# Kernel optimization log

Hardware: AMD Instinct MI355X
Metric: run time of the kernel (lower is better)

The kernel has to match this reference:

```python
import jax, jax.numpy as jnp
import numpy as np

N = 32768        # tokens (batch*seq)
D = 1024         # input_dim
E = 64           # n_experts
TOPK = 2


def setup_inputs() -> dict:
    key = jax.random.key(0)
    k_x, k_w, k_b, k_wn, k_bn = jax.random.split(key, 5)
    scale = 1.0 / np.sqrt(D)
    return {
        "x": jax.random.normal(k_x, (N, D), dtype=jnp.float32),
        "W": jax.random.uniform(k_w, (D, E), minval=-scale, maxval=scale, dtype=jnp.float32),
        "b": jax.random.uniform(k_b, (E,), minval=-scale, maxval=scale, dtype=jnp.float32),
        "W_noise": jax.random.uniform(k_wn, (D, E), minval=-scale, maxval=scale, dtype=jnp.float32),
        "b_noise": jax.random.uniform(k_bn, (E,), minval=-scale, maxval=scale, dtype=jnp.float32),
    }


def reference(x, W, b, W_noise, b_noise):
    # logits = fc(x): single Linear (router_hidden_dims=[])
    logits = x @ W + b                      # [N, E]
    # training=False (default): no noise path; fc_noise params unused
    topk_logits, topk_indices = jax.lax.top_k(logits, TOPK)  # [N, k]
    # scatter topk logits into a -inf tensor, then softmax
    mask = jnp.sum(jax.nn.one_hot(topk_indices, E, dtype=jnp.bool_), axis=-2)  # [N, E]
    sparse_logits = jnp.where(mask, logits, -jnp.inf)
    routing_probs = jax.nn.softmax(sparse_logits, axis=-1)  # zeros off-topk
    return routing_probs, topk_indices
```

## Files before the change

kernel.cpp:

```cpp
#include <hip/hip_runtime.h>
#include <cstdint>
#include <cstddef>

#define N_TOK 32768
#define DIM   1024
#define NE    64
#define RPB   64
#define KHALF 512
#define CHUNK 32
#define NCHUNK (KHALF / CHUNK)

__device__ __forceinline__ void gload16(const float* g, float* l) {
  __builtin_amdgcn_global_load_lds(
      (const __attribute__((address_space(1))) uint32_t*)g,
      (__attribute__((address_space(3))) uint32_t*)l, 16, 0, 0);
}

__global__ __launch_bounds__(512, 4) void router_kernel(
    const float* __restrict__ x, const float* __restrict__ W,
    const float* __restrict__ bias, float* __restrict__ probs,
    float* __restrict__ idxo) {
  __shared__ __align__(1024) float xs[2][2][RPB][CHUNK];
  __shared__ float  red[4][RPB][16];
  __shared__ float4 ex[4][RPB];
  __shared__ float4 ex2[RPB];

  const int tid  = threadIdx.x;
  const int lane = tid & 63;
  const int w    = __builtin_amdgcn_readfirstlane(tid >> 6);
  const int g    = w & 3;
  const int h    = w >> 2;
  const int r0   = blockIdx.x * RPB;

  auto stage = [&](int cc) {
    const int buf = cc & 1;
    float* base = &xs[h][buf][0][0];
    const int k0 = h * KHALF + cc * CHUNK;
#pragma unroll
    for (int jj = 0; jj < 2; ++jj) {
      const int j = 2 * g + jj;
      const int row = 8 * j + (lane >> 3);
      const int sq  = (lane & 7) ^ (lane >> 3);
      gload16(x + (size_t)(r0 + row) * DIM + k0 + (sq << 2),
              base + j * 256);
    }
  };

  float acc[16];
#pragma unroll
  for (int e = 0; e < 16; ++e) acc[e] = 0.0f;

  stage(0);

  for (int cc = 0; cc < NCHUNK; ++cc) {
    __syncthreads();
    if (cc + 1 < NCHUNK) stage(cc + 1);

    const int buf = cc & 1;
    const float* xb = &xs[h][buf][0][0] + lane * CHUNK;
    const float* Wc = W + (size_t)(h * KHALF + cc * CHUNK) * NE + g * 16;

    float4 xq = make_float4(0.f, 0.f, 0.f, 0.f);
#pragma unroll
    for (int kk = 0; kk < CHUNK; ++kk) {
      if ((kk & 3) == 0) {
        const int slot = (kk >> 2) ^ (lane & 7);
        xq = *(const float4*)(xb + (slot << 2));
      }
      const float xc = ((kk & 3) == 0) ? xq.x
                     : ((kk & 3) == 1) ? xq.y
                     : ((kk & 3) == 2) ? xq.z : xq.w;
      const float* Wk = Wc + (size_t)kk * NE;
#pragma unroll
      for (int e = 0; e < 16; ++e)
        acc[e] = fmaf(Wk[e], xc, acc[e]);
    }
  }

  __syncthreads();
  if (h == 1) {
#pragma unroll
    for (int q = 0; q < 4; ++q)
      *(float4*)&red[g][lane][q * 4] = make_float4(acc[q*4+0], acc[q*4+1],
                                                   acc[q*4+2], acc[q*4+3]);
  }
  __syncthreads();

  if (h == 0) {
#pragma unroll
    for (int q = 0; q < 4; ++q) {
      float4 r = *(const float4*)&red[g][lane][q * 4];
      acc[q*4+0] += r.x; acc[q*4+1] += r.y; acc[q*4+2] += r.z; acc[q*4+3] += r.w;
    }
#pragma unroll
    for (int e = 0; e < 16; ++e) acc[e] += bias[g * 16 + e];

    float v1, v2; int j1, j2;
    if (acc[1] > acc[0]) { v1 = acc[1]; j1 = 1; v2 = acc[0]; j2 = 0; }
    else                 { v1 = acc[0]; j1 = 0; v2 = acc[1]; j2 = 1; }
#pragma unroll
    for (int e = 2; e < 16; ++e) {
      if (acc[e] > v1)      { v2 = v1; j2 = j1; v1 = acc[e]; j1 = e; }
      else if (acc[e] > v2) { v2 = acc[e]; j2 = e; }
    }
    ex[g][lane] = make_float4(v1, v2, (float)(g * 16 + j1), (float)(g * 16 + j2));
  }
  __syncthreads();

  if (w == 0) {
    float4 m = ex[0][lane];
    float V1 = m.x, V2 = m.y, J1 = m.z, J2 = m.w;
#pragma unroll
    for (int gg = 1; gg < 4; ++gg) {
      float4 u = ex[gg][lane];
      if (u.x > V1) {
        bool s = (u.y > V1);
        V2 = s ? u.y : V1; J2 = s ? u.w : J1;
        V1 = u.x; J1 = u.z;
      } else if (u.x > V2) { V2 = u.x; J2 = u.z; }
    }
    const float e2 = __expf(V2 - V1);
    const float p1 = 1.0f / (1.0f + e2);
    const float p2 = e2 * p1;
    ex2[lane] = make_float4(J1, J2, p1, p2);
    float2 oi; oi.x = J1; oi.y = J2;
    *(float2*)(idxo + (size_t)(r0 + lane) * 2) = oi;
  }
  __syncthreads();

  if (h == 0) {
    float4 f = ex2[lane];
    const int ij1 = (int)f.x, ij2 = (int)f.y;
    float* op = probs + (size_t)(r0 + lane) * NE + g * 16;
#pragma unroll
    for (int q = 0; q < 4; ++q) {
      float4 o;
      const int e0 = g * 16 + q * 4;
      o.x = (e0 + 0 == ij1) ? f.z : (e0 + 0 == ij2) ? f.w : 0.0f;
      o.y = (e0 + 1 == ij1) ? f.z : (e0 + 1 == ij2) ? f.w : 0.0f;
      o.z = (e0 + 2 == ij1) ? f.z : (e0 + 2 == ij2) ? f.w : 0.0f;
      o.w = (e0 + 3 == ij1) ? f.z : (e0 + 3 == ij2) ? f.w : 0.0f;
      *(float4*)(op + q * 4) = o;
    }
  }
}

extern "C" void kernel_launch(void* const* d_in, const int* in_sizes, int n_in,
                              void* d_out, int out_size, void* d_ws, size_t ws_size,
                              hipStream_t stream) {
  (void)in_sizes; (void)n_in; (void)out_size; (void)d_ws; (void)ws_size;
  const float* x = (const float*)d_in[0];
  const float* W = (const float*)d_in[1];
  const float* b = (const float*)d_in[2];
  float* out  = (float*)d_out;
  float* idxo = out + (size_t)N_TOK * NE;

  dim3 grid(N_TOK / RPB);
  dim3 block(512);
  hipLaunchKernelGGL(router_kernel, grid, block, 0, stream, x, W, b, out, idxo);
}
```

Before: 248.2 us.

## Use 8x8 register tiles with split-K across waves and LDS-staged W

Replaces the per-lane row dot product, where each lane reads W directly from global memory, with an 8-row by 8-expert register tile per lane. Both x, transposed with an XOR swizzle, and W chunks are double-buffered in LDS, and each of the 8 waves handles a different slice of K. Partial sums are combined through a tree reduction in shared memory, and wave 0 does the top-2 selection using cross-lane shuffles. The aim is to raise FMA-to-load ratio and cut redundant W traffic. In exchange it uses 64 accumulators per lane and adds several extra barriers, which adds register pressure and may lower occupancy.

```diff
diff --git a/kernel.cpp b/kernel.cpp
--- a/kernel.cpp
+++ b/kernel.cpp
@@ -6,9 +6,8 @@
 #define DIM   1024
 #define NE    64
 #define RPB   64
-#define KHALF 512
-#define CHUNK 32
-#define NCHUNK (KHALF / CHUNK)
+#define CH    64
+#define NCH   (DIM / CH)
 
 __device__ __forceinline__ void gload16(const float* g, float* l) {
   __builtin_amdgcn_global_load_lds(
@@ -20,127 +19,193 @@
     const float* __restrict__ x, const float* __restrict__ W,
     const float* __restrict__ bias, float* __restrict__ probs,
     float* __restrict__ idxo) {
-  __shared__ __align__(1024) float xs[2][2][RPB][CHUNK];
-  __shared__ float  red[4][RPB][16];
-  __shared__ float4 ex[4][RPB];
-  __shared__ float4 ex2[RPB];
+  __shared__ __align__(1024) float smem[16384];
+  float* xT = smem;
+  float* wB = smem + 8192;
 
   const int tid  = threadIdx.x;
   const int lane = tid & 63;
   const int w    = __builtin_amdgcn_readfirstlane(tid >> 6);
-  const int g    = w & 3;
-  const int h    = w >> 2;
+  const int ri   = lane >> 3;
+  const int ei   = lane & 7;
   const int r0   = blockIdx.x * RPB;
 
-  auto stage = [&](int cc) {
+  const int srow = tid >> 3;
+  const int sq   = tid & 7;
+  const float* xrow = x + (size_t)(r0 + srow) * DIM + sq * 4;
+
+  float acc[64];
+#pragma unroll
+  for (int i = 0; i < 64; ++i) acc[i] = 0.0f;
+
+  const int rp0 = srow ^ ((sq >> 1) << 3);
+  const int rp1 = srow ^ ((((sq + 8) >> 1)) << 3);
+
+  float4 xg0 = *(const float4*)(xrow);
+  float4 xg1 = *(const float4*)(xrow + 32);
+#pragma unroll
+  for (int jj = 0; jj < 2; ++jj) {
+    const int j = w * 2 + jj;
+    gload16(W + (size_t)(j * 4) * NE + lane * 4, wB + j * 256);
+  }
+  {
+    float* xb = xT;
+    const int q1 = sq + 8;
+    xb[(sq*4+0)*64 + rp0] = xg0.x;  xb[(sq*4+1)*64 + rp0] = xg0.y;
+    xb[(sq*4+2)*64 + rp0] = xg0.z;  xb[(sq*4+3)*64 + rp0] = xg0.w;
+    xb[(q1*4+0)*64 + rp1] = xg1.x;  xb[(q1*4+1)*64 + rp1] = xg1.y;
+    xb[(q1*4+2)*64 + rp1] = xg1.z;  xb[(q1*4+3)*64 + rp1] = xg1.w;
+  }
+
+  for (int cc = 0; cc < NCH; ++cc) {
+    __syncthreads();
     const int buf = cc & 1;
-    float* base = &xs[h][buf][0][0];
-    const int k0 = h * KHALF + cc * CHUNK;
-#pragma unroll
-    for (int jj = 0; jj < 2; ++jj) {
-      const int j = 2 * g + jj;
-      const int row = 8 * j + (lane >> 3);
-      const int sq  = (lane & 7) ^ (lane >> 3);
-      gload16(x + (size_t)(r0 + row) * DIM + k0 + (sq << 2),
-              base + j * 256);
+    const int nb  = buf ^ 1;
+    const bool pf = (cc + 1 < NCH);
+
+    if (pf) {
+      const int k0n = (cc + 1) * CH;
+      xg0 = *(const float4*)(xrow + k0n);
+      xg1 = *(const float4*)(xrow + k0n + 32);
+#pragma unroll
+      for (int jj = 0; jj < 2; ++jj) {
+        const int j = w * 2 + jj;
+        gload16(W + (size_t)(k0n + j * 4) * NE + lane * 4,
+                wB + nb * 4096 + j * 256);
+      }
+    }
+
+    const float* xbr = xT + buf * 4096 + ((ri ^ w) * 8);
+    const float* wbr = wB + buf * 4096 + ei * 8;
+#pragma unroll
+    for (int i = 0; i < 8; ++i) {
+      const int kk = w * 8 + i;
+      const float4 xa = *(const float4*)(xbr + kk * 64);
+      const float4 xc = *(const float4*)(xbr + kk * 64 + 4);
+      const float4 wa = *(const float4*)(wbr + kk * 64);
+      const float4 wc = *(const float4*)(wbr + kk * 64 + 4);
+#define ROUTER_FMA_ROW(J, XS)                                   \
+      acc[(J)*8+0] = fmaf(XS, wa.x, acc[(J)*8+0]);              \
+      acc[(J)*8+1] = fmaf(XS, wa.y, acc[(J)*8+1]);              \
+      acc[(J)*8+2] = fmaf(XS, wa.z, acc[(J)*8+2]);              \
+      acc[(J)*8+3] = fmaf(XS, wa.w, acc[(J)*8+3]);              \
+      acc[(J)*8+4] = fmaf(XS, wc.x, acc[(J)*8+4]);              \
+      acc[(J)*8+5] = fmaf(XS, wc.y, acc[(J)*8+5]);              \
+      acc[(J)*8+6] = fmaf(XS, wc.z, acc[(J)*8+6]);              \
+      acc[(J)*8+7] = fmaf(XS, wc.w, acc[(J)*8+7]);
+      ROUTER_FMA_ROW(0, xa.x)
+      ROUTER_FMA_ROW(1, xa.y)
+      ROUTER_FMA_ROW(2, xa.z)
+      ROUTER_FMA_ROW(3, xa.w)
+      ROUTER_FMA_ROW(4, xc.x)
+      ROUTER_FMA_ROW(5, xc.y)
+      ROUTER_FMA_ROW(6, xc.z)
+      ROUTER_FMA_ROW(7, xc.w)
+#undef ROUTER_FMA_ROW
+    }
+
+    if (pf) {
+      float* xb = xT + nb * 4096;
+      const int q1 = sq + 8;
+      xb[(sq*4+0)*64 + rp0] = xg0.x;  xb[(sq*4+1)*64 + rp0] = xg0.y;
+      xb[(sq*4+2)*64 + rp0] = xg0.z;  xb[(sq*4+3)*64 + rp0] = xg0.w;
+      xb[(q1*4+0)*64 + rp1] = xg1.x;  xb[(q1*4+1)*64 + rp1] = xg1.y;
+      xb[(q1*4+2)*64 + rp1] = xg1.z;  xb[(q1*4+3)*64 + rp1] = xg1.w;
+    }
+  }
+
+  auto write_tile = [&](float* T) {
+#pragma unroll
+    for (int j = 0; j < 8; ++j) {
+      *(float4*)(T + (ri*8+j)*64 + ei*8) =
+          make_float4(acc[j*8+0], acc[j*8+1], acc[j*8+2], acc[j*8+3]);
+      *(float4*)(T + (ri*8+j)*64 + ei*8 + 4) =
+          make_float4(acc[j*8+4], acc[j*8+5], acc[j*8+6], acc[j*8+7]);
     }
   };
-
-  float acc[16];
-#pragma unroll
-  for (int e = 0; e < 16; ++e) acc[e] = 0.0f;
-
-  stage(0);
-
-  for (int cc = 0; cc < NCHUNK; ++cc) {
-    __syncthreads();
-    if (cc + 1 < NCHUNK) stage(cc + 1);
-
-    const int buf = cc & 1;
-    const float* xb = &xs[h][buf][0][0] + lane * CHUNK;
-    const float* Wc = W + (size_t)(h * KHALF + cc * CHUNK) * NE + g * 16;
-
-    float4 xq = make_float4(0.f, 0.f, 0.f, 0.f);
-#pragma unroll
-    for (int kk = 0; kk < CHUNK; ++kk) {
-      if ((kk & 3) == 0) {
-        const int slot = (kk >> 2) ^ (lane & 7);
-        xq = *(const float4*)(xb + (slot << 2));
-      }
-      const float xc = ((kk & 3) == 0) ? xq.x
-                     : ((kk & 3) == 1) ? xq.y
-                     : ((kk & 3) == 2) ? xq.z : xq.w;
-      const float* Wk = Wc + (size_t)kk * NE;
-#pragma unroll
-      for (int e = 0; e < 16; ++e)
-        acc[e] = fmaf(Wk[e], xc, acc[e]);
-    }
-  }
-
-  __syncthreads();
-  if (h == 1) {
-#pragma unroll
-    for (int q = 0; q < 4; ++q)
-      *(float4*)&red[g][lane][q * 4] = make_float4(acc[q*4+0], acc[q*4+1],
-                                                   acc[q*4+2], acc[q*4+3]);
-  }
-  __syncthreads();
-
-  if (h == 0) {
-#pragma unroll
-    for (int q = 0; q < 4; ++q) {
-      float4 r = *(const float4*)&red[g][lane][q * 4];
-      acc[q*4+0] += r.x; acc[q*4+1] += r.y; acc[q*4+2] += r.z; acc[q*4+3] += r.w;
-    }
-#pragma unroll
-    for (int e = 0; e < 16; ++e) acc[e] += bias[g * 16 + e];
-
-    float v1, v2; int j1, j2;
-    if (acc[1] > acc[0]) { v1 = acc[1]; j1 = 1; v2 = acc[0]; j2 = 0; }
-    else                 { v1 = acc[0]; j1 = 0; v2 = acc[1]; j2 = 1; }
-#pragma unroll
-    for (int e = 2; e < 16; ++e) {
-      if (acc[e] > v1)      { v2 = v1; j2 = j1; v1 = acc[e]; j1 = e; }
-      else if (acc[e] > v2) { v2 = acc[e]; j2 = e; }
-    }
-    ex[g][lane] = make_float4(v1, v2, (float)(g * 16 + j1), (float)(g * 16 + j2));
-  }
+  auto add_tile = [&](const float* T) {
+#pragma unroll
+    for (int j = 0; j < 8; ++j) {
+      const float4 a = *(const float4*)(T + (ri*8+j)*64 + ei*8);
+      const float4 b = *(const float4*)(T + (ri*8+j)*64 + ei*8 + 4);
+      acc[j*8+0] += a.x; acc[j*8+1] += a.y; acc[j*8+2] += a.z; acc[j*8+3] += a.w;
+      acc[j*8+4] += b.x; acc[j*8+5] += b.y; acc[j*8+6] += b.z; acc[j*8+7] += b.w;
+    }
+  };
+
+  __syncthreads();
+  if (w >= 4) write_tile(smem + (w - 4) * 4096);
+  __syncthreads();
+  if (w < 4) add_tile(smem + w * 4096);
+  __syncthreads();
+  if (w == 2 || w == 3) write_tile(smem + w * 4096);
+  __syncthreads();
+  if (w < 2) add_tile(smem + (w + 2) * 4096);
+  __syncthreads();
+  if (w == 1) write_tile(smem + 4096);
   __syncthreads();
 
   if (w == 0) {
-    float4 m = ex[0][lane];
-    float V1 = m.x, V2 = m.y, J1 = m.z, J2 = m.w;
-#pragma unroll
-    for (int gg = 1; gg < 4; ++gg) {
-      float4 u = ex[gg][lane];
-      if (u.x > V1) {
-        bool s = (u.y > V1);
-        V2 = s ? u.y : V1; J2 = s ? u.w : J1;
-        V1 = u.x; J1 = u.z;
-      } else if (u.x > V2) { V2 = u.x; J2 = u.z; }
-    }
-    const float e2 = __expf(V2 - V1);
-    const float p1 = 1.0f / (1.0f + e2);
-    const float p2 = e2 * p1;
-    ex2[lane] = make_float4(J1, J2, p1, p2);
-    float2 oi; oi.x = J1; oi.y = J2;
-    *(float2*)(idxo + (size_t)(r0 + lane) * 2) = oi;
-  }
-  __syncthreads();
-
-  if (h == 0) {
-    float4 f = ex2[lane];
-    const int ij1 = (int)f.x, ij2 = (int)f.y;
-    float* op = probs + (size_t)(r0 + lane) * NE + g * 16;
-#pragma unroll
-    for (int q = 0; q < 4; ++q) {
-      float4 o;
-      const int e0 = g * 16 + q * 4;
-      o.x = (e0 + 0 == ij1) ? f.z : (e0 + 0 == ij2) ? f.w : 0.0f;
-      o.y = (e0 + 1 == ij1) ? f.z : (e0 + 1 == ij2) ? f.w : 0.0f;
-      o.z = (e0 + 2 == ij1) ? f.z : (e0 + 2 == ij2) ? f.w : 0.0f;
-      o.w = (e0 + 3 == ij1) ? f.z : (e0 + 3 == ij2) ? f.w : 0.0f;
-      *(float4*)(op + q * 4) = o;
+    add_tile(smem + 4096);
+
+    const float4 b0 = *(const float4*)(bias + ei * 8);
+    const float4 b1 = *(const float4*)(bias + ei * 8 + 4);
+#pragma unroll
+    for (int j = 0; j < 8; ++j) {
+      acc[j*8+0] += b0.x; acc[j*8+1] += b0.y; acc[j*8+2] += b0.z; acc[j*8+3] += b0.w;
+      acc[j*8+4] += b1.x; acc[j*8+5] += b1.y; acc[j*8+6] += b1.z; acc[j*8+7] += b1.w;
+    }
+
+#pragma unroll
+    for (int j = 0; j < 8; ++j) {
+      float v1, v2, j1, j2;
+      {
+        const float a0 = acc[j*8+0], a1 = acc[j*8+1];
+        if (a1 > a0) { v1 = a1; j1 = (float)(ei*8+1); v2 = a0; j2 = (float)(ei*8+0); }
+        else         { v1 = a0; j1 = (float)(ei*8+0); v2 = a1; j2 = (float)(ei*8+1); }
+#pragma unroll
+        for (int e = 2; e < 8; ++e) {
+          const float a = acc[j*8+e]; const float jf = (float)(ei*8+e);
+          if (a > v1)      { v2 = v1; j2 = j1; v1 = a; j1 = jf; }
+          else if (a > v2) { v2 = a; j2 = jf; }
+        }
+      }
+#pragma unroll
+      for (int m = 1; m <= 4; m <<= 1) {
+        const float u1  = __shfl_xor(v1, m, 64);
+        const float uj1 = __shfl_xor(j1, m, 64);
+        const float u2  = __shfl_xor(v2, m, 64);
+        const float uj2 = __shfl_xor(j2, m, 64);
+        const bool uwin = (u1 > v1) || (u1 == v1 && uj1 < j1);
+        const float t1 = uwin ? u1 : v1,  tj1 = uwin ? uj1 : j1;
+        const float l1 = uwin ? v1 : u1,  lj1 = uwin ? j1 : uj1;
+        const float c2 = uwin ? u2 : v2,  cj2 = uwin ? uj2 : j2;
+        const bool sw = (c2 > l1) || (c2 == l1 && cj2 < lj1);
+        v1 = t1; j1 = tj1;
+        v2 = sw ? c2 : l1; j2 = sw ? cj2 : lj1;
+      }
+      const float e2 = __expf(v2 - v1);
+      const float p1 = 1.0f / (1.0f + e2);
+      const float p2 = e2 * p1;
+      const int row = r0 + ri * 8 + j;
+      const int ij1 = (int)j1, ij2 = (int)j2;
+      float* op = probs + (size_t)row * NE + ei * 8;
+      float4 o0, o1;
+      const int e0 = ei * 8;
+      o0.x = (e0+0 == ij1) ? p1 : (e0+0 == ij2) ? p2 : 0.0f;
+      o0.y = (e0+1 == ij1) ? p1 : (e0+1 == ij2) ? p2 : 0.0f;
+      o0.z = (e0+2 == ij1) ? p1 : (e0+2 == ij2) ? p2 : 0.0f;
+      o0.w = (e0+3 == ij1) ? p1 : (e0+3 == ij2) ? p2 : 0.0f;
+      o1.x = (e0+4 == ij1) ? p1 : (e0+4 == ij2) ? p2 : 0.0f;
+      o1.y = (e0+5 == ij1) ? p1 : (e0+5 == ij2) ? p2 : 0.0f;
+      o1.z = (e0+6 == ij1) ? p1 : (e0+6 == ij2) ? p2 : 0.0f;
+      o1.w = (e0+7 == ij1) ? p1 : (e0+7 == ij2) ? p2 : 0.0f;
+      *(float4*)(op) = o0;
+      *(float4*)(op + 4) = o1;
+      if (ei == 0) {
+        float2 oi; oi.x = j1; oi.y = j2;
+        *(float2*)(idxo + (size_t)row * 2) = oi;
+      }
     }
   }
 }
```

Result: slower. 288.3 us (+16.1%).

## Split experts across all waves with full-K loop and padded LDS tile

Applied to the files above, without the earlier changes.

Each of the eight waves now owns eight experts over the whole K dimension, where before K was split in halves with a cross-wave reduction. The x tile is staged as 64-column chunks into a padded pitch-68 LDS layout that replaces the XOR swizzle, and W is read as float4 vectors. Top-2 selection is rewritten as a per-row 8-lane shuffle reduction over logits written back to LDS, which removes several block barriers and lets all waves share the epilogue. This lowers per-thread accumulator count and reduction traffic, but launch bounds drop to two blocks per CU. Each lane also now handles only eight experts per x value loaded from LDS.

```diff
diff --git a/kernel.cpp b/kernel.cpp
--- a/kernel.cpp
+++ b/kernel.cpp
@@ -6,9 +6,11 @@
 #define DIM   1024
 #define NE    64
 #define RPB   64
-#define KHALF 512
-#define CHUNK 32
-#define NCHUNK (KHALF / CHUNK)
+#define CH    64
+#define NCH   (DIM / CH)
+#define PITCH 68
+#define XFLTS (RPB * PITCH)
+#define NSLICE 17
 
 __device__ __forceinline__ void gload16(const float* g, float* l) {
   __builtin_amdgcn_global_load_lds(
@@ -16,131 +18,136 @@
       (__attribute__((address_space(3))) uint32_t*)l, 16, 0, 0);
 }
 
-__global__ __launch_bounds__(512, 4) void router_kernel(
+__global__ __launch_bounds__(512, 2) void router_kernel(
     const float* __restrict__ x, const float* __restrict__ W,
     const float* __restrict__ bias, float* __restrict__ probs,
     float* __restrict__ idxo) {
-  __shared__ __align__(1024) float xs[2][2][RPB][CHUNK];
-  __shared__ float  red[4][RPB][16];
-  __shared__ float4 ex[4][RPB];
-  __shared__ float4 ex2[RPB];
+  __shared__ __align__(1024) float xs[2 * XFLTS];
 
   const int tid  = threadIdx.x;
   const int lane = tid & 63;
   const int w    = __builtin_amdgcn_readfirstlane(tid >> 6);
-  const int g    = w & 3;
-  const int h    = w >> 2;
+  const int e0   = w * 8;
   const int r0   = blockIdx.x * RPB;
 
-  auto stage = [&](int cc) {
-    const int buf = cc & 1;
-    float* base = &xs[h][buf][0][0];
-    const int k0 = h * KHALF + cc * CHUNK;
+  const float* srcs[3];
+  int dstoff[3];
+  const int nsl = (w == 0) ? 3 : 2;
+  {
+    const int js[3] = {2 * w, 2 * w + 1, 16};
 #pragma unroll
-    for (int jj = 0; jj < 2; ++jj) {
-      const int j = 2 * g + jj;
-      const int row = 8 * j + (lane >> 3);
-      const int sq  = (lane & 7) ^ (lane >> 3);
-      gload16(x + (size_t)(r0 + row) * DIM + k0 + (sq << 2),
-              base + j * 256);
+    for (int s = 0; s < 3; ++s) {
+      const int off = js[s] * 1024 + lane * 16;
+      const int row = off / 272;
+      const int rem = off % 272;
+      const int col = (rem >= 256) ? 0 : (rem >> 2);
+      srcs[s]   = x + (size_t)(r0 + row) * DIM + col;
+      dstoff[s] = js[s] * 256;
+    }
+  }
+  auto stage = [&](int buf) {
+    float* base = xs + buf * XFLTS;
+#pragma unroll
+    for (int s = 0; s < 3; ++s) {
+      if (s < nsl) {
+        gload16(srcs[s], base + dstoff[s]);
+        srcs[s] += CH;
+      }
     }
   };
 
-  float acc[16];
+  float acc[8];
 #pragma unroll
-  for (int e = 0; e < 16; ++e) acc[e] = 0.0f;
+  for (int e = 0; e < 8; ++e) acc[e] = 0.0f;
 
   stage(0);
 
-  for (int cc = 0; cc < NCHUNK; ++cc) {
+  for (int cc = 0; cc < NCH; ++cc) {
     __syncthreads();
-    if (cc + 1 < NCHUNK) stage(cc + 1);
+    if (cc + 1 < NCH) stage((cc + 1) & 1);
 
-    const int buf = cc & 1;
-    const float* xb = &xs[h][buf][0][0] + lane * CHUNK;
-    const float* Wc = W + (size_t)(h * KHALF + cc * CHUNK) * NE + g * 16;
+    const float* xb = xs + (cc & 1) * XFLTS + lane * PITCH;
+    const float* Wc = W + (size_t)(cc * CH) * NE + e0;
 
-    float4 xq = make_float4(0.f, 0.f, 0.f, 0.f);
 #pragma unroll
-    for (int kk = 0; kk < CHUNK; ++kk) {
-      if ((kk & 3) == 0) {
-        const int slot = (kk >> 2) ^ (lane & 7);
-        xq = *(const float4*)(xb + (slot << 2));
-      }
-      const float xc = ((kk & 3) == 0) ? xq.x
-                     : ((kk & 3) == 1) ? xq.y
-                     : ((kk & 3) == 2) ? xq.z : xq.w;
-      const float* Wk = Wc + (size_t)kk * NE;
-#pragma unroll
-      for (int e = 0; e < 16; ++e)
-        acc[e] = fmaf(Wk[e], xc, acc[e]);
+    for (int g = 0; g < 8; ++g) {
+      const float4 xq0 = *(const float4*)(xb + g * 8);
+      const float4 xq1 = *(const float4*)(xb + g * 8 + 4);
+#define KKSTEP(KK, XS)                                              \
+      { const float4 wa = *(const float4*)(Wc + (g * 8 + KK) * NE); \
+        const float4 wb = *(const float4*)(Wc + (g * 8 + KK) * NE + 4); \
+        acc[0] = fmaf(XS, wa.x, acc[0]); acc[1] = fmaf(XS, wa.y, acc[1]); \
+        acc[2] = fmaf(XS, wa.z, acc[2]); acc[3] = fmaf(XS, wa.w, acc[3]); \
+        acc[4] = fmaf(XS, wb.x, acc[4]); acc[5] = fmaf(XS, wb.y, acc[5]); \
+        acc[6] = fmaf(XS, wb.z, acc[6]); acc[7] = fmaf(XS, wb.w, acc[7]); }
+      KKSTEP(0, xq0.x) KKSTEP(1, xq0.y) KKSTEP(2, xq0.z) KKSTEP(3, xq0.w)
+      KKSTEP(4, xq1.x) KKSTEP(5, xq1.y) KKSTEP(6, xq1.z) KKSTEP(7, xq1.w)
+#undef KKSTEP
     }
   }
 
-  __syncthreads();
-  if (h == 1) {
-#pragma unroll
-    for (int q = 0; q < 4; ++q)
-      *(float4*)&red[g][lane][q * 4] = make_float4(acc[q*4+0], acc[q*4+1],
-                                                   acc[q*4+2], acc[q*4+3]);
+  {
+    const float4 b03 = *(const float4*)(bias + e0);
+    const float4 b47 = *(const float4*)(bias + e0 + 4);
+    float* lg = xs + lane * PITCH + e0;
+    *(float4*)(lg)     = make_float4(acc[0] + b03.x, acc[1] + b03.y,
+                                     acc[2] + b03.z, acc[3] + b03.w);
+    *(float4*)(lg + 4) = make_float4(acc[4] + b47.x, acc[5] + b47.y,
+                                     acc[6] + b47.z, acc[7] + b47.w);
   }
   __syncthreads();
 
-  if (h == 0) {
+  {
+    const int row = w * 8 + (lane >> 3);
+    const int oct = lane & 7;
+    const float* lr = xs + row * PITCH + oct * 8;
+    const float4 A = *(const float4*)(lr);
+    const float4 B = *(const float4*)(lr + 4);
+    const float av[8] = {A.x, A.y, A.z, A.w, B.x, B.y, B.z, B.w};
+
+    float v1, v2, j1, j2;
+    if (av[1] > av[0]) { v1 = av[1]; j1 = (float)(oct*8+1); v2 = av[0]; j2 = (float)(oct*8+0); }
+    else               { v1 = av[0]; j1 = (float)(oct*8+0); v2 = av[1]; j2 = (float)(oct*8+1); }
 #pragma unroll
-    for (int q = 0; q < 4; ++q) {
-      float4 r = *(const float4*)&red[g][lane][q * 4];
-      acc[q*4+0] += r.x; acc[q*4+1] += r.y; acc[q*4+2] += r.z; acc[q*4+3] += r.w;
+    for (int e = 2; e < 8; ++e) {
+      const float a = av[e]; const float jf = (float)(oct*8+e);
+      if (a > v1)      { v2 = v1; j2 = j1; v1 = a; j1 = jf; }
+      else if (a > v2) { v2 = a; j2 = jf; }
     }
 #pragma unroll
-    for (int e = 0; e < 16; ++e) acc[e] += bias[g * 16 + e];
-
-    float v1, v2; int j1, j2;
-    if (acc[1] > acc[0]) { v1 = acc[1]; j1 = 1; v2 = acc[0]; j2 = 0; }
-    else                 { v1 = acc[0]; j1 = 0; v2 = acc[1]; j2 = 1; }
-#pragma unroll
-    for (int e = 2; e < 16; ++e) {
-      if (acc[e] > v1)      { v2 = v1; j2 = j1; v1 = acc[e]; j1 = e; }
-      else if (acc[e] > v2) { v2 = acc[e]; j2 = e; }
+    for (int m = 1; m <= 4; m <<= 1) {
+      const float u1  = __shfl_xor(v1, m, 64);
+      const float uj1 = __shfl_xor(j1, m, 64);
+      const float u2  = __shfl_xor(v2, m, 64);
+      const float uj2 = __shfl_xor(j2, m, 64);
+      const bool uwin = (u1 > v1) || (u1 == v1 && uj1 < j1);
+      const float t1 = uwin ? u1 : v1,  tj1 = uwin ? uj1 : j1;
+      const float l1 = uwin ? v1 : u1,  lj1 = uwin ? j1 : uj1;
+      const float c2 = uwin ? u2 : v2,  cj2 = uwin ? uj2 : j2;
+      const bool sw = (c2 > l1) || (c2 == l1 && cj2 < lj1);
+      v1 = t1; j1 = tj1;
+      v2 = sw ? c2 : l1; j2 = sw ? cj2 : lj1;
     }
-    ex[g][lane] = make_float4(v1, v2, (float)(g * 16 + j1), (float)(g * 16 + j2));
-  }
-  __syncthreads();
-
-  if (w == 0) {
-    float4 m = ex[0][lane];
-    float V1 = m.x, V2 = m.y, J1 = m.z, J2 = m.w;
-#pragma unroll
-    for (int gg = 1; gg < 4; ++gg) {
-      float4 u = ex[gg][lane];
-      if (u.x > V1) {
-        bool s = (u.y > V1);
-        V2 = s ? u.y : V1; J2 = s ? u.w : J1;
-        V1 = u.x; J1 = u.z;
-      } else if (u.x > V2) { V2 = u.x; J2 = u.z; }
-    }
-    const float e2 = __expf(V2 - V1);
-    const float p1 = 1.0f / (1.0f + e2);
-    const float p2 = e2 * p1;
-    ex2[lane] = make_float4(J1, J2, p1, p2);
-    float2 oi; oi.x = J1; oi.y = J2;
-    *(float2*)(idxo + (size_t)(r0 + lane) * 2) = oi;
-  }
-  __syncthreads();
-
-  if (h == 0) {
-    float4 f = ex2[lane];
-    const int ij1 = (int)f.x, ij2 = (int)f.y;
-    float* op = probs + (size_t)(r0 + lane) * NE + g * 16;
-#pragma unroll
-    for (int q = 0; q < 4; ++q) {
-      float4 o;
-      const int e0 = g * 16 + q * 4;
-      o.x = (e0 + 0 == ij1) ? f.z : (e0 + 0 == ij2) ? f.w : 0.0f;
-      o.y = (e0 + 1 == ij1) ? f.z : (e0 + 1 == ij2) ? f.w : 0.0f;
-      o.z = (e0 + 2 == ij1) ? f.z : (e0 + 2 == ij2) ? f.w : 0.0f;
-      o.w = (e0 + 3 == ij1) ? f.z : (e0 + 3 == ij2) ? f.w : 0.0f;
-      *(float4*)(op + q * 4) = o;
+    const float ex = __expf(v2 - v1);
+    const float p1 = 1.0f / (1.0f + ex);
+    const float p2 = ex * p1;
+    const int ij1 = (int)j1, ij2 = (int)j2;
+    float* op = probs + (size_t)(r0 + row) * NE + oct * 8;
+    float4 o0, o1;
+    const int eb = oct * 8;
+    o0.x = (eb+0 == ij1) ? p1 : (eb+0 == ij2) ? p2 : 0.0f;
+    o0.y = (eb+1 == ij1) ? p1 : (eb+1 == ij2) ? p2 : 0.0f;
+    o0.z = (eb+2 == ij1) ? p1 : (eb+2 == ij2) ? p2 : 0.0f;
+    o0.w = (eb+3 == ij1) ? p1 : (eb+3 == ij2) ? p2 : 0.0f;
+    o1.x = (eb+4 == ij1) ? p1 : (eb+4 == ij2) ? p2 : 0.0f;
+    o1.y = (eb+5 == ij1) ? p1 : (eb+5 == ij2) ? p2 : 0.0f;
+    o1.z = (eb+6 == ij1) ? p1 : (eb+6 == ij2) ? p2 : 0.0f;
+    o1.w = (eb+7 == ij1) ? p1 : (eb+7 == ij2) ? p2 : 0.0f;
+    *(float4*)(op)     = o0;
+    *(float4*)(op + 4) = o1;
+    if (oct == 0) {
+      float2 oi; oi.x = j1; oi.y = j2;
+      *(float2*)(idxo + (size_t)(r0 + row) * 2) = oi;
     }
   }
 }
```

New measurement: 288.4 us. +16.2%, slower.
